# Kernel tuning notes

Measured on AMD Instinct MI355X. Metric: run time of the kernel, lower is better.

The kernel has to match this reference:

```python
import jax, jax.numpy as jnp
import numpy as np

N = 100000      # nodes
E = 1600000     # edges (avg degree 16)
IN_DIM = 64
OUT_DIM = 128
BN_EPS = 1e-5


def setup_inputs() -> dict:
    key = jax.random.key(0)
    kx, ke, kw, kb, ks = jax.random.split(key, 5)
    x = jax.random.normal(kx, (N, IN_DIM), dtype=jnp.float32)
    edge_index = jax.random.randint(ke, (2, E), 0, N, dtype=jnp.int32)
    # GCNConv linear weight (no bias inside lin; conv bias separate)
    W = jax.random.normal(kw, (IN_DIM, OUT_DIM), dtype=jnp.float32) / np.sqrt(IN_DIM)
    bias = jax.random.normal(kb, (OUT_DIM,), dtype=jnp.float32) * 0.01
    # skip projection Linear(in_dim, out_dim, bias=False)
    skip_W = jax.random.normal(ks, (IN_DIM, OUT_DIM), dtype=jnp.float32) / np.sqrt(IN_DIM)
    # BatchNorm1d affine params (training-mode batch stats used in forward)
    gamma = jnp.ones((OUT_DIM,), dtype=jnp.float32)
    beta = jnp.zeros((OUT_DIM,), dtype=jnp.float32)
    return {"x": x, "edge_index": edge_index, "W": W, "bias": bias,
            "skip_W": skip_W, "gamma": gamma, "beta": beta}


def _gcn_forward(x, edge_index, W, bias, skip_W, gamma, beta):
    n = x.shape[0]
    # GCNConv, normalize=True, add_self_loops=True (PyG defaults)
    row, col = edge_index[0], edge_index[1]
    loop = jnp.arange(n, dtype=edge_index.dtype)
    row_f = jnp.concatenate([row, loop])   # source nodes
    col_f = jnp.concatenate([col, loop])   # target nodes

    xt = x @ W                             # [N, OUT]
    deg = jax.ops.segment_sum(jnp.ones_like(col_f, dtype=xt.dtype), col_f,
                              num_segments=n)          # >= 1 due to self loops
    dinv = jax.lax.rsqrt(deg)
    norm = dinv[row_f] * dinv[col_f]                    # [E+N]
    msgs = xt[row_f] * norm[:, None]                    # gather + scale
    out = jax.ops.segment_sum(msgs, col_f, num_segments=n) + bias

    # skip-sum (in_dim != out_dim -> project)
    out = out + x @ skip_W

    # BatchNorm1d (training-mode batch statistics), affine
    mean = out.mean(axis=0)
    var = out.var(axis=0)
    out = (out - mean) * jax.lax.rsqrt(var + BN_EPS) * gamma + beta

    # ReLU; dropout p=0.0 -> identity
    return jax.nn.relu(out)


def reference(x, edge_index, W, bias, skip_W, gamma, beta):
    return _gcn_forward(x, edge_index, W, bias, skip_W, gamma, beta)
```

## Files before the change

kernel.cpp:

```cpp
#include <hip/hip_runtime.h>


typedef unsigned short ushort;
typedef __bf16 bf16x8 __attribute__((ext_vector_type(8)));
typedef float f32x4 __attribute__((ext_vector_type(4)));
typedef float f32x2 __attribute__((ext_vector_type(2)));
typedef ushort u16x8 __attribute__((ext_vector_type(8)));

constexpr int N_NODES = 100000;
constexpr int N_PAD   = 100096;
constexpr int E_EDGES = 1600000;

constexpr int BUCK_SHIFT = 7;
constexpr int NBUCK   = (N_NODES + 127) / 128;
constexpr int NBUCK_P = 784;
constexpr int CHUNK   = 8192;
constexpr int NCHUNK  = (E_EDGES + CHUNK - 1) / CHUNK;
constexpr int GH_STRIDE = 200;
constexpr int SORT_CAP = 4096;

constexpr size_t OFF_SCALE  = 0;
constexpr size_t OFF_DINV   = 256;
constexpr size_t OFF_ROWPTR = 100352;
constexpr size_t OFF_BASE   = 200480;
constexpr size_t OFF_GHIST  = 201280;
constexpr size_t OFF_BINNED = 358080;
constexpr size_t OFF_PART   = OFF_BINNED;
constexpr size_t OFF_A      = 1958080;
constexpr size_t OFF_PRE    = 8364224;
constexpr size_t OFF_XD8    = OFF_PRE;
constexpr size_t OFF_BT     = 14770368;
constexpr size_t OFF_TICK   = 14778560;

static __device__ __forceinline__ ushort f2bf(float f) {
    union { float f; unsigned u; } v; v.f = f;
    unsigned r = v.u + 0x7FFFu + ((v.u >> 16) & 1u);
    return (ushort)(r >> 16);
}
static __device__ __forceinline__ float bf2f(ushort u) {
    union { unsigned u; float f; } v; v.u = (unsigned)u << 16;
    return v.f;
}
static __device__ __forceinline__ unsigned pack_fp8x4(float a, float b, float c, float d) {
    int r = 0;
    r = __builtin_amdgcn_cvt_pk_fp8_f32(a, b, r, false);
    r = __builtin_amdgcn_cvt_pk_fp8_f32(c, d, r, true);
    return (unsigned)r;
}

__global__ __launch_bounds__(256) void k_hist(const int* __restrict__ col,
                                              int* __restrict__ gh_t,
                                              const float* __restrict__ W,
                                              const float* __restrict__ skipW,
                                              ushort* __restrict__ Bt,
                                              unsigned* __restrict__ tick) {
    int c = blockIdx.x, t = threadIdx.x;
    if (c >= NCHUNK) {
        int idx = (c - NCHUNK) * 256 + t;
        if (c == NCHUNK && t < 2) tick[t] = 0u;
        int k = idx >> 7, n = idx & 127;
        float v = (k < 64) ? W[k * 128 + n] : skipW[(k - 64) * 128 + n];
        Bt[n * 128 + k] = f2bf(v);
        return;
    }
    __shared__ int h[NBUCK_P];
    for (int b = t; b < NBUCK_P; b += 256) h[b] = 0;
    __syncthreads();
    const int4* col4 = (const int4*)col;
    int g0 = c * (CHUNK / 4);
#pragma unroll
    for (int i = 0; i < CHUNK / 1024; ++i) {
        int g4 = g0 + i * 256 + t;
        if (g4 * 4 + 3 < E_EDGES) {
            int4 cc = col4[g4];
            atomicAdd(&h[cc.x >> BUCK_SHIFT], 1);
            atomicAdd(&h[cc.y >> BUCK_SHIFT], 1);
            atomicAdd(&h[cc.z >> BUCK_SHIFT], 1);
            atomicAdd(&h[cc.w >> BUCK_SHIFT], 1);
        } else {
#pragma unroll
            for (int j = 0; j < 4; ++j) {
                int e = g4 * 4 + j;
                if (e < E_EDGES) atomicAdd(&h[col[e] >> BUCK_SHIFT], 1);
            }
        }
    }
    __syncthreads();
    for (int b = t; b < NBUCK_P; b += 256) gh_t[(size_t)b * GH_STRIDE + c] = h[b];
}

__global__ __launch_bounds__(256) void k_scan(int* __restrict__ gh_t,
                                              int* __restrict__ base,
                                              int* __restrict__ rowptr,
                                              unsigned* __restrict__ tick) {
    __shared__ int wtot[4];
    __shared__ int amlast;
    int w = threadIdx.x >> 6, l = threadIdx.x & 63;
    int b = blockIdx.x * 4 + w;
    int* rowp = gh_t + (size_t)b * GH_STRIDE;
    int carry = 0;
#pragma unroll
    for (int i = 0; i < 4; ++i) {
        int idx = i * 64 + l;
        int v = (idx < NCHUNK) ? rowp[idx] : 0;
        int orig = v;
#pragma unroll
        for (int d = 1; d < 64; d <<= 1) {
            int o = __shfl_up(v, d);
            if (l >= d) v += o;
        }
        if (idx < NCHUNK) rowp[idx] = carry + v - orig;
        carry += __shfl(v, 63);
    }
    if (l == 0 && b < NBUCK) atomicExch(&base[b], carry);
    __syncthreads();
    if (threadIdx.x == 0)
        amlast = (atomicAdd(tick + 0, 1u) == (unsigned)(gridDim.x - 1)) ? 1 : 0;
    __syncthreads();
    if (!amlast) return;

    int t = threadIdx.x;
    int i0 = t * 4;
    int v0 = (i0 + 0 < NBUCK) ? atomicAdd(&base[i0 + 0], 0) : 0;
    int v1 = (i0 + 1 < NBUCK) ? atomicAdd(&base[i0 + 1], 0) : 0;
    int v2 = (i0 + 2 < NBUCK) ? atomicAdd(&base[i0 + 2], 0) : 0;
    int v3 = (i0 + 3 < NBUCK) ? atomicAdd(&base[i0 + 3], 0) : 0;
    int s = v0 + v1 + v2 + v3;
    int incl = s;
#pragma unroll
    for (int d = 1; d < 64; d <<= 1) {
        int o = __shfl_up(incl, d);
        if (l >= d) incl += o;
    }
    if (l == 63) wtot[w] = incl;
    __syncthreads();
    int wpre = 0;
    for (int ww = 0; ww < w; ++ww) wpre += wtot[ww];
    int excl = wpre + incl - s;
    if (i0 + 0 < NBUCK) base[i0 + 0] = excl;
    if (i0 + 1 < NBUCK) base[i0 + 1] = excl + v0;
    if (i0 + 2 < NBUCK) base[i0 + 2] = excl + v0 + v1;
    if (i0 + 3 < NBUCK) base[i0 + 3] = excl + v0 + v1 + v2;
    if (t == 255) {
        int total = wpre + incl;
        base[NBUCK] = total;
        rowptr[N_NODES] = total;
    }
}

__global__ __launch_bounds__(256) void k_scatter_bin(const int* __restrict__ row,
                                                     const int* __restrict__ col,
                                                     const int* __restrict__ gh_t,
                                                     const int* __restrict__ base,
                                                     unsigned int* __restrict__ binned) {
    __shared__ int cur[NBUCK_P];
    int c = blockIdx.x, t = threadIdx.x;
    for (int b = t; b < NBUCK_P; b += 256) {
        int bb = (b < NBUCK) ? base[b] : 0;
        cur[b] = bb + gh_t[(size_t)b * GH_STRIDE + c];
    }
    __syncthreads();
    const int4* col4 = (const int4*)col;
    const int4* row4 = (const int4*)row;
    int g0 = c * (CHUNK / 4);
#pragma unroll
    for (int i = 0; i < CHUNK / 1024; ++i) {
        int g4 = g0 + i * 256 + t;
        if (g4 * 4 + 3 < E_EDGES) {
            int4 cc = col4[g4];
            int4 rr = row4[g4];
            int p;
            p = atomicAdd(&cur[cc.x >> BUCK_SHIFT], 1);
            binned[p] = ((unsigned)(cc.x & 127) << 17) | (unsigned)rr.x;
            p = atomicAdd(&cur[cc.y >> BUCK_SHIFT], 1);
            binned[p] = ((unsigned)(cc.y & 127) << 17) | (unsigned)rr.y;
            p = atomicAdd(&cur[cc.z >> BUCK_SHIFT], 1);
            binned[p] = ((unsigned)(cc.z & 127) << 17) | (unsigned)rr.z;
            p = atomicAdd(&cur[cc.w >> BUCK_SHIFT], 1);
            binned[p] = ((unsigned)(cc.w & 127) << 17) | (unsigned)rr.w;
        } else {
#pragma unroll
            for (int j = 0; j < 4; ++j) {
                int e = g4 * 4 + j;
                if (e < E_EDGES) {
                    int d = col[e], s = row[e];
                    int p = atomicAdd(&cur[d >> BUCK_SHIFT], 1);
                    binned[p] = ((unsigned)(d & 127) << 17) | (unsigned)s;
                }
            }
        }
    }
}

__global__ __launch_bounds__(256) void k_sortbucket(unsigned int* __restrict__ binned,
                                                    const int* __restrict__ base,
                                                    int* __restrict__ rowptr,
                                                    float* __restrict__ dinv,
                                                    const float* __restrict__ x,
                                                    unsigned* __restrict__ xd8,
                                                    ushort* __restrict__ A) {
    __shared__ unsigned int ebuf[SORT_CAP];
    __shared__ int sbuf[SORT_CAP];
    __shared__ int lcnt[128];
    __shared__ int lptr[128];
    __shared__ float ldinv[128];
    __shared__ int wsum[2];
    int b = blockIdx.x, t = threadIdx.x;
    int i0 = base[b], i1 = base[b + 1];
    int cnt = i1 - i0;
    if (cnt > SORT_CAP) cnt = SORT_CAP;
    int n0 = b << BUCK_SHIFT;
    int nn = min(128, N_NODES - n0);

    for (int k = t; k < cnt; k += 256) ebuf[k] = binned[i0 + k];
    if (t < 128) lcnt[t] = 0;
    __syncthreads();
    for (int k = t; k < cnt; k += 256) atomicAdd(&lcnt[ebuf[k] >> 17], 1);
    __syncthreads();

    int myc = 0, val = 0;
    if (t < 128) {
        myc = lcnt[t];
        val = myc;
#pragma unroll
        for (int d = 1; d < 64; d <<= 1) {
            int o = __shfl_up(val, d);
            if ((t & 63) >= d) val += o;
        }
        if ((t & 63) == 63) wsum[t >> 6] = val;
    }
    __syncthreads();
    if (t < 128) {
        if (t >= 64) val += wsum[0];
        int excl = val - myc;
        lptr[t] = excl;
        float dv = rsqrtf((float)myc + 1.0f);
        ldinv[t] = dv;
        if (t < nn) {
            rowptr[n0 + t] = i0 + excl;
            dinv[n0 + t] = dv;
        }
    }
    __syncthreads();
    for (int k = t; k < cnt; k += 256) {
        unsigned int e = ebuf[k];
        int j = (int)(e >> 17);
        int p = atomicAdd(&lptr[j], 1);
        sbuf[p] = (int)(e & 0x1FFFF);
    }
    __syncthreads();
    for (int k = t; k < cnt; k += 256) binned[i0 + k] = (unsigned int)sbuf[k];

#pragma unroll
    for (int it = 0; it < 8; ++it) {
        int idx = it * 256 + t;
        int nl = idx >> 4, q = idx & 15;
        int c = n0 + nl;
        unsigned w8 = 0;
        ushort4 xb = {0, 0, 0, 0};
        if (nl < nn) {
            float4 v = ((const float4*)x)[(size_t)c * 16 + q];
            float d = ldinv[nl];
            w8 = pack_fp8x4(v.x * d, v.y * d, v.z * d, v.w * d);
            xb.x = f2bf(v.x); xb.y = f2bf(v.y); xb.z = f2bf(v.z); xb.w = f2bf(v.w);
        }
        xd8[(size_t)c * 16 + q] = w8;
        ((ushort4*)A)[(size_t)c * 32 + 16 + q] = xb;
    }
}

__global__ __launch_bounds__(256) void k_agg(const unsigned* __restrict__ xd8,
                                             const float* __restrict__ dinv,
                                             const int* __restrict__ rowptr,
                                             const unsigned int* __restrict__ csr,
                                             ushort* __restrict__ A) {
    int t = blockIdx.x * blockDim.x + threadIdx.x;
    if (t >= N_PAD * 16) return;
    int c = t >> 4;
    int q = t & 15;
    if (c >= N_NODES) {
        ushort4 z = {0, 0, 0, 0};
        ((ushort4*)A)[(size_t)c * 32 + q] = z;
        return;
    }
    float dc = dinv[c];
    float4 acc;
    {
        unsigned w = xd8[t];
        f32x2 lo = __builtin_amdgcn_cvt_pk_f32_fp8((int)w, false);
        f32x2 hi = __builtin_amdgcn_cvt_pk_f32_fp8((int)w, true);
        acc.x = lo.x; acc.y = lo.y; acc.z = hi.x; acc.w = hi.y;
    }
    int i0 = rowptr[c], i1 = rowptr[c + 1];
    int i = i0;
    for (; i + 8 <= i1; i += 8) {
        int s[8];
#pragma unroll
        for (int k = 0; k < 8; ++k) s[k] = (int)csr[i + k];
        unsigned w[8];
#pragma unroll
        for (int k = 0; k < 8; ++k) w[k] = xd8[s[k] * 16 + q];
#pragma unroll
        for (int k = 0; k < 8; ++k) {
            f32x2 lo = __builtin_amdgcn_cvt_pk_f32_fp8((int)w[k], false);
            f32x2 hi = __builtin_amdgcn_cvt_pk_f32_fp8((int)w[k], true);
            acc.x += lo.x; acc.y += lo.y; acc.z += hi.x; acc.w += hi.y;
        }
    }
    for (; i < i1; ++i) {
        unsigned w = xd8[(int)csr[i] * 16 + q];
        f32x2 lo = __builtin_amdgcn_cvt_pk_f32_fp8((int)w, false);
        f32x2 hi = __builtin_amdgcn_cvt_pk_f32_fp8((int)w, true);
        acc.x += lo.x; acc.y += lo.y; acc.z += hi.x; acc.w += hi.y;
    }
    ushort4 o;
    o.x = f2bf(acc.x * dc); o.y = f2bf(acc.y * dc);
    o.z = f2bf(acc.z * dc); o.w = f2bf(acc.w * dc);
    ((ushort4*)A)[(size_t)c * 32 + q] = o;
}

__global__ __launch_bounds__(512) void k_gemm(const ushort* __restrict__ A,
                                              const ushort* __restrict__ Bt,
                                              const float* __restrict__ bias,
                                              ushort* __restrict__ pre,
                                              float* __restrict__ partial) {
    __shared__ float sred[128];
    __shared__ float qred[128];
    int tid = threadIdx.x;
    int wave = tid >> 6, lane = tid & 63;
    int wm = wave >> 2, wn = wave & 3;
    int l15 = lane & 15, quad = lane >> 4;
    int row0 = blockIdx.x * 128 + wm * 64;
    int col0 = wn * 32;

    if (tid < 128) { sred[tid] = 0.f; qred[tid] = 0.f; }
    __syncthreads();

    bf16x8 af[4][4], bf_[4][2];
#pragma unroll
    for (int kc = 0; kc < 4; ++kc) {
        int ko = kc * 32 + quad * 8;
#pragma unroll
        for (int im = 0; im < 4; ++im)
            af[kc][im] = *(const bf16x8*)&A[(size_t)(row0 + im * 16 + l15) * 128 + ko];
#pragma unroll
        for (int jn = 0; jn < 2; ++jn)
            bf_[kc][jn] = *(const bf16x8*)&Bt[(size_t)(col0 + jn * 16 + l15) * 128 + ko];
    }

    f32x4 acc[4][2];
#pragma unroll
    for (int a = 0; a < 4; ++a)
#pragma unroll
        for (int b = 0; b < 2; ++b) acc[a][b] = (f32x4){0.f, 0.f, 0.f, 0.f};

#pragma unroll
    for (int kc = 0; kc < 4; ++kc)
#pragma unroll
        for (int im = 0; im < 4; ++im)
#pragma unroll
            for (int jn = 0; jn < 2; ++jn)
                acc[im][jn] = __builtin_amdgcn_mfma_f32_16x16x32_bf16(
                    af[kc][im], bf_[kc][jn], acc[im][jn], 0, 0, 0);

    int coln[2];
    float bi[2];
#pragma unroll
    for (int jn = 0; jn < 2; ++jn) {
        coln[jn] = col0 + jn * 16 + l15;
        bi[jn] = bias[coln[jn]];
    }
    float lsum[2] = {0.f, 0.f};
    float lsq[2]  = {0.f, 0.f};
#pragma unroll
    for (int im = 0; im < 4; ++im) {
        int rbase = row0 + im * 16 + quad * 4;
#pragma unroll
        for (int r = 0; r < 4; ++r) {
            int rowi = rbase + r;
            if (rowi < N_NODES) {
#pragma unroll
                for (int jn = 0; jn < 2; ++jn) {
                    float v = acc[im][jn][r] + bi[jn];
                    pre[(size_t)rowi * 128 + coln[jn]] = f2bf(v);
                    lsum[jn] += v;
                    lsq[jn]  += v * v;
                }
            }
        }
    }
#pragma unroll
    for (int jn = 0; jn < 2; ++jn) {
        atomicAdd(&sred[coln[jn]], lsum[jn]);
        atomicAdd(&qred[coln[jn]], lsq[jn]);
    }
    __syncthreads();
    if (tid < 128) {
        partial[(size_t)blockIdx.x * 256 + tid]       = sred[tid];
        partial[(size_t)blockIdx.x * 256 + 128 + tid] = qred[tid];
    }
}

__global__ __launch_bounds__(256) void k_reduce(const float* __restrict__ partial,
                                                const float* __restrict__ gamma,
                                                const float* __restrict__ beta,
                                                float* __restrict__ scaleshift) {
    __shared__ float ls[256], lq[256];
    int j = blockIdx.x;
    int t = threadIdx.x;
    float s = 0.f, q = 0.f;
    for (int p = t; p < NBUCK; p += 256) {
        s += partial[(size_t)p * 256 + j];
        q += partial[(size_t)p * 256 + 128 + j];
    }
    ls[t] = s; lq[t] = q;
    __syncthreads();
#pragma unroll
    for (int off = 128; off > 0; off >>= 1) {
        if (t < off) { ls[t] += ls[t + off]; lq[t] += lq[t + off]; }
        __syncthreads();
    }
    if (t == 0) {
        float mean = ls[0] * (1.0f / N_NODES);
        float var  = lq[0] * (1.0f / N_NODES) - mean * mean;
        float sc   = gamma[j] * rsqrtf(var + 1e-5f);
        scaleshift[j]       = sc;
        scaleshift[128 + j] = beta[j] - mean * sc;
    }
}

__global__ __launch_bounds__(256) void k_apply(const ushort* __restrict__ pre,
                                               float* __restrict__ out,
                                               const float* __restrict__ ss) {
    int t = blockIdx.x * blockDim.x + threadIdx.x;
    if (t >= N_NODES * 16) return;
    int j8 = t & 15;
    u16x8 p = ((const u16x8*)pre)[t];
    float4 sc0 = ((const float4*)ss)[j8 * 2];
    float4 sc1 = ((const float4*)ss)[j8 * 2 + 1];
    float4 sh0 = ((const float4*)(ss + 128))[j8 * 2];
    float4 sh1 = ((const float4*)(ss + 128))[j8 * 2 + 1];
    float4 v0, v1;
    v0.x = fmaxf(fmaf(bf2f(p[0]), sc0.x, sh0.x), 0.f);
    v0.y = fmaxf(fmaf(bf2f(p[1]), sc0.y, sh0.y), 0.f);
    v0.z = fmaxf(fmaf(bf2f(p[2]), sc0.z, sh0.z), 0.f);
    v0.w = fmaxf(fmaf(bf2f(p[3]), sc0.w, sh0.w), 0.f);
    v1.x = fmaxf(fmaf(bf2f(p[4]), sc1.x, sh1.x), 0.f);
    v1.y = fmaxf(fmaf(bf2f(p[5]), sc1.y, sh1.y), 0.f);
    v1.z = fmaxf(fmaf(bf2f(p[6]), sc1.z, sh1.z), 0.f);
    v1.w = fmaxf(fmaf(bf2f(p[7]), sc1.w, sh1.w), 0.f);
    ((float4*)out)[t * 2]     = v0;
    ((float4*)out)[t * 2 + 1] = v1;
}

extern "C" void kernel_launch(void* const* d_in, const int* in_sizes, int n_in,
                              void* d_out, int out_size, void* d_ws, size_t ws_size,
                              hipStream_t stream) {
    const float* x      = (const float*)d_in[0];
    const int*   eidx   = (const int*)d_in[1];
    const float* W      = (const float*)d_in[2];
    const float* bias   = (const float*)d_in[3];
    const float* skipW  = (const float*)d_in[4];
    const float* gamma  = (const float*)d_in[5];
    const float* beta   = (const float*)d_in[6];
    float* out = (float*)d_out;
    float* ws  = (float*)d_ws;

    const int* row = eidx;
    const int* col = eidx + E_EDGES;

    float* scaleshift = ws + OFF_SCALE;
    float* dinv       = ws + OFF_DINV;
    int*   rowptr     = (int*)(ws + OFF_ROWPTR);
    int*   base       = (int*)(ws + OFF_BASE);
    int*   gh_t      = (int*)(ws + OFF_GHIST);
    unsigned int* binned = (unsigned int*)(ws + OFF_BINNED);
    float* partial    = ws + OFF_PART;
    ushort* A         = (ushort*)(ws + OFF_A);
    unsigned* xd8     = (unsigned*)(ws + OFF_XD8);
    ushort* pre       = (ushort*)(ws + OFF_PRE);
    ushort* Bt        = (ushort*)(ws + OFF_BT);
    unsigned* tick    = (unsigned*)(ws + OFF_TICK);

    k_hist<<<NCHUNK + 64, 256, 0, stream>>>(col, gh_t, W, skipW, Bt, tick);
    k_scan<<<NBUCK_P / 4, 256, 0, stream>>>(gh_t, base, rowptr, tick);
    k_scatter_bin<<<NCHUNK, 256, 0, stream>>>(row, col, gh_t, base, binned);
    k_sortbucket<<<NBUCK, 256, 0, stream>>>(binned, base, rowptr, dinv, x, xd8, A);
    k_agg<<<(N_PAD * 16 + 255) / 256, 256, 0, stream>>>(xd8, dinv, rowptr, binned, A);
    k_gemm<<<NBUCK, 512, 0, stream>>>(A, Bt, bias, pre, partial);
    k_reduce<<<128, 256, 0, stream>>>(partial, gamma, beta, scaleshift);
    k_apply<<<(N_NODES * 16 + 255) / 256, 256, 0, stream>>>(pre, out, scaleshift);
}
```

Measured before the change: 215.2 us.

## Make GEMM persistent over 256 blocks, transpose MFMA output, drop bias before BatchNorm

The GEMM kernel now runs a fixed grid of 256 blocks. Each block loops over row tiles and loads the B fragments once. The MFMA operands are swapped so each lane holds four consecutive columns, which allows vectorized ushort4 stores to the pre-activation buffer. Per-column sums are reduced with wave shuffles before the LDS atomics, and the reduce kernel only reads 256 partials. The bias add is dropped because BatchNorm cancels it. This also shifts the stored pre values by the constant bias, which the normalization absorbs.

```diff
diff --git a/kernel.cpp b/kernel.cpp
--- a/kernel.cpp
+++ b/kernel.cpp
@@ -18,6 +18,7 @@
 constexpr int NCHUNK  = (E_EDGES + CHUNK - 1) / CHUNK;
 constexpr int GH_STRIDE = 200;
 constexpr int SORT_CAP = 4096;
+constexpr int GG      = 256;
 
 constexpr size_t OFF_SCALE  = 0;
 constexpr size_t OFF_DINV   = 256;
@@ -319,80 +320,94 @@
     ((ushort4*)A)[(size_t)c * 32 + q] = o;
 }
 
-__global__ __launch_bounds__(512) void k_gemm(const ushort* __restrict__ A,
-                                              const ushort* __restrict__ Bt,
-                                              const float* __restrict__ bias,
-                                              ushort* __restrict__ pre,
-                                              float* __restrict__ partial) {
+__global__ __launch_bounds__(512, 2) void k_gemm(const ushort* __restrict__ A,
+                                                 const ushort* __restrict__ Bt,
+                                                 ushort* __restrict__ pre,
+                                                 float* __restrict__ partial) {
     __shared__ float sred[128];
     __shared__ float qred[128];
     int tid = threadIdx.x;
     int wave = tid >> 6, lane = tid & 63;
     int wm = wave >> 2, wn = wave & 3;
     int l15 = lane & 15, quad = lane >> 4;
-    int row0 = blockIdx.x * 128 + wm * 64;
     int col0 = wn * 32;
 
     if (tid < 128) { sred[tid] = 0.f; qred[tid] = 0.f; }
     __syncthreads();
 
-    bf16x8 af[4][4], bf_[4][2];
-#pragma unroll
-    for (int kc = 0; kc < 4; ++kc) {
-        int ko = kc * 32 + quad * 8;
-#pragma unroll
-        for (int im = 0; im < 4; ++im)
-            af[kc][im] = *(const bf16x8*)&A[(size_t)(row0 + im * 16 + l15) * 128 + ko];
-#pragma unroll
-        for (int jn = 0; jn < 2; ++jn)
-            bf_[kc][jn] = *(const bf16x8*)&Bt[(size_t)(col0 + jn * 16 + l15) * 128 + ko];
-    }
-
-    f32x4 acc[4][2];
-#pragma unroll
-    for (int a = 0; a < 4; ++a)
-#pragma unroll
-        for (int b = 0; b < 2; ++b) acc[a][b] = (f32x4){0.f, 0.f, 0.f, 0.f};
-
+    bf16x8 bf_[4][2];
 #pragma unroll
     for (int kc = 0; kc < 4; ++kc)
 #pragma unroll
-        for (int im = 0; im < 4; ++im)
-#pragma unroll
-            for (int jn = 0; jn < 2; ++jn)
-                acc[im][jn] = __builtin_amdgcn_mfma_f32_16x16x32_bf16(
-                    af[kc][im], bf_[kc][jn], acc[im][jn], 0, 0, 0);
-
-    int coln[2];
-    float bi[2];
-#pragma unroll
-    for (int jn = 0; jn < 2; ++jn) {
-        coln[jn] = col0 + jn * 16 + l15;
-        bi[jn] = bias[coln[jn]];
-    }
-    float lsum[2] = {0.f, 0.f};
-    float lsq[2]  = {0.f, 0.f};
-#pragma unroll
-    for (int im = 0; im < 4; ++im) {
-        int rbase = row0 + im * 16 + quad * 4;
-#pragma unroll
-        for (int r = 0; r < 4; ++r) {
-            int rowi = rbase + r;
-            if (rowi < N_NODES) {
-#pragma unroll
-                for (int jn = 0; jn < 2; ++jn) {
-                    float v = acc[im][jn][r] + bi[jn];
-                    pre[(size_t)rowi * 128 + coln[jn]] = f2bf(v);
-                    lsum[jn] += v;
-                    lsq[jn]  += v * v;
+        for (int jc = 0; jc < 2; ++jc)
+            bf_[kc][jc] = *(const bf16x8*)&Bt[(size_t)(col0 + jc * 16 + l15) * 128 + kc * 32 + quad * 8];
+
+    float lsum[8] = {0.f, 0.f, 0.f, 0.f, 0.f, 0.f, 0.f, 0.f};
+    float lsq[8]  = {0.f, 0.f, 0.f, 0.f, 0.f, 0.f, 0.f, 0.f};
+
+    for (int ci = blockIdx.x; ci < NBUCK; ci += GG) {
+        int row0 = ci * 128 + wm * 64;
+        bf16x8 af[4][4];
+#pragma unroll
+        for (int kc = 0; kc < 4; ++kc)
+#pragma unroll
+            for (int ir = 0; ir < 4; ++ir)
+                af[kc][ir] = *(const bf16x8*)&A[(size_t)(row0 + ir * 16 + l15) * 128 + kc * 32 + quad * 8];
+
+        f32x4 acc[4][2];
+#pragma unroll
+        for (int ir = 0; ir < 4; ++ir)
+#pragma unroll
+            for (int jc = 0; jc < 2; ++jc) acc[ir][jc] = (f32x4){0.f, 0.f, 0.f, 0.f};
+
+#pragma unroll
+        for (int kc = 0; kc < 4; ++kc)
+#pragma unroll
+            for (int ir = 0; ir < 4; ++ir)
+#pragma unroll
+                for (int jc = 0; jc < 2; ++jc)
+                    acc[ir][jc] = __builtin_amdgcn_mfma_f32_16x16x32_bf16(
+                        bf_[kc][jc], af[kc][ir], acc[ir][jc], 0, 0, 0);
+
+#pragma unroll
+        for (int ir = 0; ir < 4; ++ir) {
+            int row = row0 + ir * 16 + l15;
+            bool live = row < N_NODES;
+#pragma unroll
+            for (int jc = 0; jc < 2; ++jc) {
+                ushort4 o;
+                o.x = f2bf(acc[ir][jc][0]); o.y = f2bf(acc[ir][jc][1]);
+                o.z = f2bf(acc[ir][jc][2]); o.w = f2bf(acc[ir][jc][3]);
+                *(ushort4*)&pre[(size_t)row * 128 + col0 + jc * 16 + quad * 4] = o;
+                if (live) {
+#pragma unroll
+                    for (int r = 0; r < 4; ++r) {
+                        float v = acc[ir][jc][r];
+                        lsum[jc * 4 + r] += v;
+                        lsq[jc * 4 + r]  += v * v;
+                    }
                 }
             }
         }
     }
-#pragma unroll
-    for (int jn = 0; jn < 2; ++jn) {
-        atomicAdd(&sred[coln[jn]], lsum[jn]);
-        atomicAdd(&qred[coln[jn]], lsq[jn]);
+
+#pragma unroll
+    for (int m = 1; m < 16; m <<= 1) {
+#pragma unroll
+        for (int i = 0; i < 8; ++i) {
+            lsum[i] += __shfl_xor(lsum[i], m);
+            lsq[i]  += __shfl_xor(lsq[i], m);
+        }
+    }
+    if (l15 == 0) {
+#pragma unroll
+        for (int jc = 0; jc < 2; ++jc)
+#pragma unroll
+            for (int r = 0; r < 4; ++r) {
+                int c = col0 + jc * 16 + quad * 4 + r;
+                atomicAdd(&sred[c], lsum[jc * 4 + r]);
+                atomicAdd(&qred[c], lsq[jc * 4 + r]);
+            }
     }
     __syncthreads();
     if (tid < 128) {
@@ -409,7 +424,7 @@
     int j = blockIdx.x;
     int t = threadIdx.x;
     float s = 0.f, q = 0.f;
-    for (int p = t; p < NBUCK; p += 256) {
+    for (int p = t; p < GG; p += 256) {
         s += partial[(size_t)p * 256 + j];
         q += partial[(size_t)p * 256 + 128 + j];
     }
@@ -459,10 +474,9 @@
     const float* x      = (const float*)d_in[0];
     const int*   eidx   = (const int*)d_in[1];
     const float* W      = (const float*)d_in[2];
-    const float* bias   = (const float*)d_in[3];
-    const float* skipW  = (const float*)d_in[4];
     const float* gamma  = (const float*)d_in[5];
     const float* beta   = (const float*)d_in[6];
+    const float* skipW  = (const float*)d_in[4];
     float* out = (float*)d_out;
     float* ws  = (float*)d_ws;
 
@@ -473,7 +487,7 @@
     float* dinv       = ws + OFF_DINV;
     int*   rowptr     = (int*)(ws + OFF_ROWPTR);
     int*   base       = (int*)(ws + OFF_BASE);
-    int*   gh_t      = (int*)(ws + OFF_GHIST);
+    int*   gh_t       = (int*)(ws + OFF_GHIST);
     unsigned int* binned = (unsigned int*)(ws + OFF_BINNED);
     float* partial    = ws + OFF_PART;
     ushort* A         = (ushort*)(ws + OFF_A);
@@ -487,7 +501,7 @@
     k_scatter_bin<<<NCHUNK, 256, 0, stream>>>(row, col, gh_t, base, binned);
     k_sortbucket<<<NBUCK, 256, 0, stream>>>(binned, base, rowptr, dinv, x, xd8, A);
     k_agg<<<(N_PAD * 16 + 255) / 256, 256, 0, stream>>>(xd8, dinv, rowptr, binned, A);
-    k_gemm<<<NBUCK, 512, 0, stream>>>(A, Bt, bias, pre, partial);
+    k_gemm<<<GG, 512, 0, stream>>>(A, Bt, pre, partial);
     k_reduce<<<128, 256, 0, stream>>>(partial, gamma, beta, scaleshift);
     k_apply<<<(N_NODES * 16 + 255) / 256, 256, 0, stream>>>(pre, out, scaleshift);
 }
```

Result: faster. 197.2 us (-8.3%).
